# Performance work log

Measured on AMD Instinct MI355X. Metric: run time of the kernel, lower is better.

The kernel has to match this reference:

```python
import jax, jax.numpy as jnp
import numpy as np

DATA_SIZE = 16
OUT_DIM = 2 * DATA_SIZE  # predict_uncertainty=True
T = 128
BATCH = 4
L = 6368       # flattened root-MLP param count
H1 = 2133      # GradualMLP hidden 1: int(2/3*16 + 1/3*6368)
H2 = 4250      # GradualMLP hidden 2: int(1/3*16 + 2/3*6368)
FORCING_PROB = 1.0


def setup_inputs() -> dict:
    key = jax.random.key(0)
    k = jax.random.split(key, 8)
    xs = jax.random.normal(k[0], (BATCH, T, DATA_SIZE), jnp.float32)
    ts = jnp.broadcast_to(jnp.linspace(0.0, 1.0, T, dtype=jnp.float32), (BATCH, T))
    # A initialized near identity (module uses eye); small noise keeps the scan non-trivial but stable
    A = jnp.eye(L, dtype=jnp.float32) * 0.999 + 1e-4 * jax.random.normal(k[1], (L, L), jnp.float32)
    Bm = 0.01 * jax.random.normal(k[2], (L, DATA_SIZE + 1), jnp.float32)
    W1 = jax.random.normal(k[3], (H1, DATA_SIZE), jnp.float32) / np.float32(np.sqrt(DATA_SIZE))
    b1 = jnp.zeros((H1,), jnp.float32)
    W2 = jax.random.normal(k[4], (H2, H1), jnp.float32) / np.float32(np.sqrt(H1))
    b2 = jnp.zeros((H2,), jnp.float32)
    W3 = jax.random.normal(k[5], (L, H2), jnp.float32) / np.float32(np.sqrt(H2))
    b3 = jnp.zeros((L,), jnp.float32)
    return {"xs": xs, "ts": ts, "A": A, "Bm": Bm, "W1": W1, "b1": b1,
            "W2": W2, "b2": b2, "W3": W3, "b3": b3, "seed": 0}


def _root_apply(theta, tin):
    # unflatten theta into MLP(1 -> 64 -> 64 -> 32) params, in eqx leaf order (w, b per layer)
    w0 = theta[0:64].reshape(64, 1);      c0 = theta[64:128]
    w1 = theta[128:4224].reshape(64, 64); c1 = theta[4224:4288]
    w2 = theta[4288:6336].reshape(32, 64); c2 = theta[6336:6368]
    h = jax.nn.relu(w0 @ tin + c0)
    h = jaxax_relu = jax.nn.relu(w1 @ h + c1)
    out = w2 @ h + c2
    mean, std = jnp.split(out, 2)
    return jnp.concatenate([jnp.tanh(mean), jax.nn.softplus(std)])  # (OUT_DIM,)


def _forward_seq(xs_, ts_, k_, A, Bm, W1, b1, W2, b2, W3, b3):
    # theta_init = GradualMLP(data_size -> L) applied to xs_[0]
    h = jax.nn.relu(W1 @ xs_[0] + b1)
    h = jax.nn.relu(W2 @ h + b2)
    theta0 = W3 @ h + b3  # (L,)
    keys = jax.random.split(k_, xs_.shape[0])

    def f(carry, inp):
        thet, x_hat, x_prev, t_prev = carry
        x_true, t_curr, key = inp  # t_curr: (1,)
        delta_t = t_curr - t_prev
        x_t = jnp.where(jax.random.bernoulli(key, FORCING_PROB), x_true, x_hat)
        diff = jnp.concatenate([t_curr, x_t]) - jnp.concatenate([t_prev, x_prev])  # time_as_channel
        thet_next = A @ thet + Bm @ diff
        x_next = _root_apply(thet_next, t_curr + delta_t)
        return (thet_next, x_next[:DATA_SIZE], x_hat, t_curr), x_next

    _, xs_hat = jax.lax.scan(f, (theta0, xs_[0], xs_[0], ts_[0:1]), (xs_, ts_[:, None], keys))
    return xs_hat  # (T, OUT_DIM)


def reference(xs, ts, A, Bm, W1, b1, W2, b2, W3, b3, seed):
    ks = jax.random.split(jax.random.key(seed), xs.shape[0])
    fwd = lambda x_, t_, k_: _forward_seq(x_, t_, k_, A, Bm, W1, b1, W2, b2, W3, b3)
    return jax.vmap(fwd)(xs, ts, ks)  # (BATCH, T, OUT_DIM)
```

## Files before the change

### kernel.cpp

```cpp
#include <hip/hip_runtime.h>
#include <cmath>

#define T_STEPS 128
#define B_SZ    4
#define L_DIM   6368
#define L4V     1592
#define NCH     4
#define CH_SL   1592
#define CH_J    398
#define H1_DIM  2133
#define H2_DIM  4250
#define NBLK    256
#define NMV     255
#define NPAIR   3184

#define OFF_THA  0
#define OFF_THB  25472
#define OFF_W1T  50944
#define OFF_W2T  83712
#define OFF_DIFF 100096
#define OFF_H1   100236
#define OFF_H2   108768
#define OFF_CTR  125824

typedef __attribute__((address_space(1))) void gvoid;
typedef __attribute__((address_space(3))) void lvoid;

__device__ __forceinline__ void fma4(float4& acc, float4 a, float4 t0, float4 t1, float4 t2, float4 t3) {
    acc.x += a.x*t0.x + a.y*t1.x + a.z*t2.x + a.w*t3.x;
    acc.y += a.x*t0.y + a.y*t1.y + a.z*t2.y + a.w*t3.y;
    acc.z += a.x*t0.z + a.y*t1.z + a.z*t2.z + a.w*t3.z;
    acc.w += a.x*t0.w + a.y*t1.w + a.z*t2.w + a.w*t3.w;
}

__device__ __forceinline__ float4 red4(float4 v) {
    #pragma unroll
    for (int off = 32; off; off >>= 1) {
        v.x += __shfl_xor(v.x, off);
        v.y += __shfl_xor(v.y, off);
        v.z += __shfl_xor(v.z, off);
        v.w += __shfl_xor(v.w, off);
    }
    return v;
}

__device__ __forceinline__ void aux_write(float4* w1o, float4* w2o, int r, float4 v) {
    if (r >= 128 && r < 4224) {
        int j = r - 128;
        w1o[(j & 63)*64 + (j >> 6)] = v;
    } else if (r >= 4288 && r < 6336) {
        int j = r - 4288;
        w2o[(j & 63)*32 + (j >> 6)] = v;
    }
}

__device__ __forceinline__ float softplusf(float x) {
    return (x > 20.f) ? x : log1pf(expf(x));
}

__device__ __forceinline__ void grid_barrier(unsigned* ctr, int myc, unsigned it1) {
    __syncthreads();
    if (threadIdx.x == 0) {
        __threadfence();
        unsigned old = __hip_atomic_fetch_add(&ctr[myc*32], 1u,
                           __ATOMIC_RELAXED, __HIP_MEMORY_SCOPE_AGENT);
        if (old == it1*32u - 1u) {
            unsigned o2 = __hip_atomic_fetch_add(&ctr[8*32], 1u,
                              __ATOMIC_RELAXED, __HIP_MEMORY_SCOPE_AGENT);
            if (o2 == it1*8u - 1u) {
                #pragma unroll
                for (int c2 = 0; c2 < 8; ++c2)
                    __hip_atomic_store(&ctr[(9 + c2)*32], it1,
                        __ATOMIC_RELAXED, __HIP_MEMORY_SCOPE_AGENT);
            }
        }
        while (__hip_atomic_load(&ctr[(9 + myc)*32],
                   __ATOMIC_RELAXED, __HIP_MEMORY_SCOPE_AGENT) < it1)
            __builtin_amdgcn_s_sleep(8);
        __threadfence();
    }
    __syncthreads();
}

__device__ __forceinline__ void stage_issue(const float4* __restrict__ src, float4* dst,
                                            int w, int l, float4& tailv) {
    #pragma unroll
    for (int k = 0; k < 3; ++k) {
        const int p = k*512 + w*64 + l;
        const int q = p ^ ((p >> 3) & 7);
        __builtin_amdgcn_global_load_lds((gvoid*)(src + q),
                                         (lvoid*)(dst + k*512 + w*64), 16, 0, 0);
    }
    const int p = 1536 + w*7 + l;
    if (l < 7) tailv = src[p ^ ((p >> 3) & 7)];
}

__device__ __forceinline__ void stage_tail(float4* dst, int w, int l, float4 tailv) {
    if (l < 7) dst[1536 + w*7 + l] = tailv;
}

template<bool HB>
__device__ __forceinline__ void chunk_fma(const float4* __restrict__ a0, const float4* __restrict__ a1,
                                          const float4* __restrict__ c0, const float4* __restrict__ c1,
                                          const float4* __restrict__ sbuf, int jg0, int l,
                                          float4& A0, float4& A1, float4& B0, float4& B1)
{
    #pragma unroll
    for (int m = 0; m < 6; ++m) {
        const int jj = m*64 + l;
        const int jg = jg0 + jj;
        float4 av0 = a0[jg], av1 = a1[jg];
        float4 bv0, bv1;
        if (HB) { bv0 = c0[jg]; bv1 = c1[jg]; }
        const int sw = (jj >> 1) & 7;
        float4 t0 = sbuf[(4*jj + 0) ^ sw];
        float4 t1 = sbuf[(4*jj + 1) ^ sw];
        float4 t2 = sbuf[(4*jj + 2) ^ sw];
        float4 t3 = sbuf[(4*jj + 3) ^ sw];
        fma4(A0, av0, t0, t1, t2, t3);
        fma4(A1, av1, t0, t1, t2, t3);
        if (HB) {
            fma4(B0, bv0, t0, t1, t2, t3);
            fma4(B1, bv1, t0, t1, t2, t3);
        }
    }
    if (l < 14) {
        const int jj = 384 + l;
        const int jg = jg0 + jj;
        float4 av0 = a0[jg], av1 = a1[jg];
        float4 bv0, bv1;
        if (HB) { bv0 = c0[jg]; bv1 = c1[jg]; }
        const int sw = (jj >> 1) & 7;
        float4 t0 = sbuf[(4*jj + 0) ^ sw];
        float4 t1 = sbuf[(4*jj + 1) ^ sw];
        float4 t2 = sbuf[(4*jj + 2) ^ sw];
        float4 t3 = sbuf[(4*jj + 3) ^ sw];
        fma4(A0, av0, t0, t1, t2, t3);
        fma4(A1, av1, t0, t1, t2, t3);
        if (HB) {
            fma4(B0, bv0, t0, t1, t2, t3);
            fma4(B1, bv1, t0, t1, t2, t3);
        }
    }
}

__global__ __launch_bounds__(512, 2)
void seq_kernel(const float* __restrict__ A,
                const float* __restrict__ Bm,
                const float* __restrict__ xs,
                const float* __restrict__ ts,
                float* __restrict__ outp,
                float* thetaA, float* thetaB,
                float* w1t, float* w2t, float* diffb,
                unsigned* ctr)
{
    __shared__ float4 sth[2*CH_SL];
    const int blk = blockIdx.x;
    const int tid = threadIdx.x;
    const int w = tid >> 6, l = tid & 63;
    const int myc = blk & 7;
    const float4* A4 = (const float4*)A;

    if (blk < NMV) {
        const int p0 = (blk * NPAIR) / NMV;
        const int p1 = ((blk + 1) * NPAIR) / NMV;
        const int pA = p0 + w;
        const int pB = pA + 8;
        const bool hasB = pB < p1;
        const int rA = pA * 2;
        const int rB = pB * 2;
        const float4* a0 = A4 + (size_t)rA * L4V;
        const float4* a1 = a0 + L4V;
        const float4* c0 = A4 + (size_t)rB * L4V;
        const float4* c1 = c0 + L4V;

        float bmA0 = 0.f, bmA1 = 0.f, bmB0 = 0.f, bmB1 = 0.f;
        if (l < 17) {
            bmA0 = Bm[rA*17 + l];
            bmA1 = Bm[(rA + 1)*17 + l];
            if (hasB) { bmB0 = Bm[rB*17 + l]; bmB1 = Bm[(rB + 1)*17 + l]; }
        }

        for (int it = 0; it < T_STEPS; ++it) {
            const float4* thIn4 = (const float4*)((it & 1) ? thetaB : thetaA);
            float4* thOut4 = (float4*)((it & 1) ? thetaA : thetaB);
            float4* w1o = (float4*)(w1t + ((it + 1) & 1) * 16384);
            float4* w2o = (float4*)(w2t + ((it + 1) & 1) * 8192);
            const float* dvec = diffb + (it & 1) * 68;

            float e0 = 0.f, e1 = 0.f, e2 = 0.f, e3 = 0.f;
            if (l < 17) { e0 = dvec[l]; e1 = dvec[17 + l]; e2 = dvec[34 + l]; e3 = dvec[51 + l]; }
            float4 A0 = make_float4(bmA0*e0, bmA0*e1, bmA0*e2, bmA0*e3);
            float4 A1 = make_float4(bmA1*e0, bmA1*e1, bmA1*e2, bmA1*e3);
            float4 B0 = make_float4(bmB0*e0, bmB0*e1, bmB0*e2, bmB0*e3);
            float4 B1 = make_float4(bmB1*e0, bmB1*e1, bmB1*e2, bmB1*e3);

            float4 tailv;
            stage_issue(thIn4, sth, w, l, tailv);
            stage_tail(sth, w, l, tailv);
            __syncthreads();

            for (int c = 0; c < NCH; ++c) {
                if (c + 1 < NCH)
                    stage_issue(thIn4 + (c + 1)*CH_SL, sth + ((c + 1) & 1)*CH_SL, w, l, tailv);
                const float4* sbuf = sth + (c & 1)*CH_SL;
                if (hasB) chunk_fma<true >(a0, a1, c0, c1, sbuf, c*CH_J, l, A0, A1, B0, B1);
                else      chunk_fma<false>(a0, a1, c0, c1, sbuf, c*CH_J, l, A0, A1, B0, B1);
                if (c + 1 < NCH) {
                    stage_tail(sth + ((c + 1) & 1)*CH_SL, w, l, tailv);
                    __syncthreads();
                }
            }

            A0 = red4(A0); A1 = red4(A1);
            if (hasB) { B0 = red4(B0); B1 = red4(B1); }
            if (l == 0) {
                thOut4[rA]     = A0;  aux_write(w1o, w2o, rA,     A0);
                thOut4[rA + 1] = A1;  aux_write(w1o, w2o, rA + 1, A1);
                if (hasB) {
                    thOut4[rB]     = B0;  aux_write(w1o, w2o, rB,     B0);
                    thOut4[rB + 1] = B1;  aux_write(w1o, w2o, rB + 1, B1);
                }
            }
            grid_barrier(ctr, myc, (unsigned)(it + 1));
        }
    } else {
        const int b = w;
        for (int it = 0; it <= T_STEPS; ++it) {
            float xv = 0.f;
            if (b < B_SZ) {
                if (it >= 1) {
                    const int t = it - 1;
                    const float* th  = (it & 1) ? thetaB : thetaA;
                    const float* w1c = w1t + (it & 1) * 16384;
                    const float* w2c = w2t + (it & 1) * 8192;
                    float tcur = ts[b*T_STEPS + t];
                    float tin = (t >= 1) ? (2.f*tcur - ts[b*T_STEPS + t - 1]) : tcur;
                    float h0 = fmaxf(th[l*4 + b] * tin + th[(64 + l)*4 + b], 0.f);
                    float a1v = th[(4224 + l)*4 + b];
                    #pragma unroll
                    for (int k = 0; k < 64; ++k)
                        a1v += w1c[(k*64 + l)*4 + b] * __shfl(h0, k);
                    float h1 = fmaxf(a1v, 0.f);
                    float ov = th[(6336 + (l & 31))*4 + b];
                    #pragma unroll
                    for (int k = 0; k < 64; ++k)
                        ov += w2c[(k*32 + (l & 31))*4 + b] * __shfl(h1, k);
                    if (l < 32) {
                        xv = (l < 16) ? tanhf(ov) : softplusf(ov);
                        outp[(b*T_STEPS + t)*32 + l] = xv;
                    }
                }
                if (it + 1 <= T_STEPS - 1) {
                    float* dd = diffb + ((it + 1) & 1) * 68 + b*17;
                    if (l < 16) {
                        float xprev = (it >= 1) ? xv : xs[(size_t)(b*T_STEPS)*16 + l];
                        dd[1 + l] = xs[(size_t)(b*T_STEPS + it + 1)*16 + l] - xprev;
                    } else if (l == 16) {
                        dd[0] = ts[b*T_STEPS + it + 1] - ts[b*T_STEPS + it];
                    }
                }
            }
            if (it < T_STEPS) grid_barrier(ctr, myc, (unsigned)(it + 1));
        }
    }
}

__global__ __launch_bounds__(256)
void init_h1(const float* __restrict__ xs, const float* __restrict__ W1,
             const float* __restrict__ b1, float* __restrict__ h1ws,
             float* __restrict__ diffb, unsigned* __restrict__ ctr)
{
    const int b = blockIdx.y;
    const int r = blockIdx.x * 256 + threadIdx.x;
    if (blockIdx.x == 0 && b == 0) {
        if (threadIdx.x < 136) diffb[threadIdx.x] = 0.f;
        for (int z = threadIdx.x; z < 576; z += 256) ctr[z] = 0u;
    }
    if (r < H1_DIM) {
        const float* wr = W1 + r*16;
        const float* x0 = xs + (size_t)b * T_STEPS * 16;
        float s = b1[r];
        #pragma unroll
        for (int k = 0; k < 16; ++k) s += wr[k] * x0[k];
        h1ws[b*H1_DIM + r] = fmaxf(s, 0.f);
    }
}

__global__ __launch_bounds__(256)
void init_mm(const float* __restrict__ W, const float* __restrict__ bias,
             const float* __restrict__ in, float* __restrict__ outp,
             int rows, int K, int dorelu, int ilv)
{
    const int w = threadIdx.x >> 6, l = threadIdx.x & 63;
    const int gw = blockIdx.x * 4 + w;
    const int nw = gridDim.x * 4;
    for (int r = gw; r < rows; r += nw) {
        const float* wr = W + (size_t)r * K;
        float a0 = 0.f, a1 = 0.f, a2 = 0.f, a3 = 0.f;
        for (int k = l; k < K; k += 64) {
            float wv = wr[k];
            a0 += wv * in[k];
            a1 += wv * in[K + k];
            a2 += wv * in[2*K + k];
            a3 += wv * in[3*K + k];
        }
        #pragma unroll
        for (int off = 32; off; off >>= 1) {
            a0 += __shfl_xor(a0, off);
            a1 += __shfl_xor(a1, off);
            a2 += __shfl_xor(a2, off);
            a3 += __shfl_xor(a3, off);
        }
        if (l == 0) {
            float bb = bias[r];
            a0 += bb; a1 += bb; a2 += bb; a3 += bb;
            if (dorelu) {
                a0 = fmaxf(a0, 0.f); a1 = fmaxf(a1, 0.f);
                a2 = fmaxf(a2, 0.f); a3 = fmaxf(a3, 0.f);
            }
            if (ilv) {
                outp[r*4 + 0] = a0; outp[r*4 + 1] = a1;
                outp[r*4 + 2] = a2; outp[r*4 + 3] = a3;
            } else {
                outp[0*rows + r] = a0; outp[1*rows + r] = a1;
                outp[2*rows + r] = a2; outp[3*rows + r] = a3;
            }
        }
    }
}

extern "C" void kernel_launch(void* const* d_in, const int* in_sizes, int n_in,
                              void* d_out, int out_size, void* d_ws, size_t ws_size,
                              hipStream_t stream) {
    const float* xs = (const float*)d_in[0];
    const float* ts = (const float*)d_in[1];
    const float* A  = (const float*)d_in[2];
    const float* Bm = (const float*)d_in[3];
    const float* W1 = (const float*)d_in[4];
    const float* b1 = (const float*)d_in[5];
    const float* W2 = (const float*)d_in[6];
    const float* b2 = (const float*)d_in[7];
    const float* W3 = (const float*)d_in[8];
    const float* b3 = (const float*)d_in[9];
    float* outp = (float*)d_out;
    float* wsf  = (float*)d_ws;

    float* thetaA = wsf + OFF_THA;
    float* thetaB = wsf + OFF_THB;
    float* w1t    = wsf + OFF_W1T;
    float* w2t    = wsf + OFF_W2T;
    float* diffb  = wsf + OFF_DIFF;
    float* h1ws   = wsf + OFF_H1;
    float* h2ws   = wsf + OFF_H2;
    unsigned* ctr = (unsigned*)(wsf + OFF_CTR);

    init_h1<<<dim3((H1_DIM + 255)/256, B_SZ), 256, 0, stream>>>(xs, W1, b1, h1ws, diffb, ctr);
    init_mm<<<dim3(128), 256, 0, stream>>>(W2, b2, h1ws, h2ws, H2_DIM, H1_DIM, 1, 0);
    init_mm<<<dim3(256), 256, 0, stream>>>(W3, b3, h2ws, thetaA, L_DIM, H2_DIM, 0, 1);
    seq_kernel<<<dim3(NBLK), dim3(512), 0, stream>>>(A, Bm, xs, ts, outp,
                                                     thetaA, thetaB, w1t, w2t, diffb, ctr);
}
```

Before: 5.041 ms.

## Software-pipeline A-row loads across chunks with register prefetch and two larger theta stages

Restructures the per-step matvec so theta is staged in two halves instead of four chunks, which removes two block barriers per step. Each thread keeps six float4 A-row values per row in registers and reloads the next group while doing the current FMAs, so global loads overlap with compute, including across time steps. The tail columns of each row are loaded once before the loop and kept in registers. Launch bounds drop to one block per CU because of the higher register use, and the grid-barrier spin sleep is shortened.

```diff
diff --git a/kernel.cpp b/kernel.cpp
--- a/kernel.cpp
+++ b/kernel.cpp
@@ -5,9 +5,8 @@
 #define B_SZ    4
 #define L_DIM   6368
 #define L4V     1592
-#define NCH     4
-#define CH_SL   1592
-#define CH_J    398
+#define CH_SL   3184
+#define CH_J    796
 #define H1_DIM  2133
 #define H2_DIM  4250
 #define NBLK    256
@@ -76,75 +75,91 @@
         }
         while (__hip_atomic_load(&ctr[(9 + myc)*32],
                    __ATOMIC_RELAXED, __HIP_MEMORY_SCOPE_AGENT) < it1)
-            __builtin_amdgcn_s_sleep(8);
+            __builtin_amdgcn_s_sleep(2);
         __threadfence();
     }
     __syncthreads();
 }
 
 __device__ __forceinline__ void stage_issue(const float4* __restrict__ src, float4* dst,
-                                            int w, int l, float4& tailv) {
+                                            int tid, int w, int l, float4& tailv) {
     #pragma unroll
-    for (int k = 0; k < 3; ++k) {
+    for (int k = 0; k < 6; ++k) {
         const int p = k*512 + w*64 + l;
         const int q = p ^ ((p >> 3) & 7);
         __builtin_amdgcn_global_load_lds((gvoid*)(src + q),
                                          (lvoid*)(dst + k*512 + w*64), 16, 0, 0);
     }
-    const int p = 1536 + w*7 + l;
-    if (l < 7) tailv = src[p ^ ((p >> 3) & 7)];
-}
-
-__device__ __forceinline__ void stage_tail(float4* dst, int w, int l, float4 tailv) {
-    if (l < 7) dst[1536 + w*7 + l] = tailv;
+    const int p = 3072 + tid;
+    if (tid < 112) tailv = src[p ^ ((p >> 3) & 7)];
+}
+
+__device__ __forceinline__ void stage_tail(float4* dst, int tid, float4 tailv) {
+    if (tid < 112) dst[3072 + tid] = tailv;
 }
 
 template<bool HB>
-__device__ __forceinline__ void chunk_fma(const float4* __restrict__ a0, const float4* __restrict__ a1,
-                                          const float4* __restrict__ c0, const float4* __restrict__ c1,
-                                          const float4* __restrict__ sbuf, int jg0, int l,
-                                          float4& A0, float4& A1, float4& B0, float4& B1)
+__device__ __forceinline__ void load6(const float4* __restrict__ a0, const float4* __restrict__ a1,
+                                      const float4* __restrict__ c0, const float4* __restrict__ c1,
+                                      int jg0, int l,
+                                      float4 (&r0)[6], float4 (&r1)[6],
+                                      float4 (&s0)[6], float4 (&s1)[6])
 {
     #pragma unroll
     for (int m = 0; m < 6; ++m) {
-        const int jj = m*64 + l;
-        const int jg = jg0 + jj;
-        float4 av0 = a0[jg], av1 = a1[jg];
-        float4 bv0, bv1;
-        if (HB) { bv0 = c0[jg]; bv1 = c1[jg]; }
+        const int jg = jg0 + m*64 + l;
+        r0[m] = a0[jg]; r1[m] = a1[jg];
+        if (HB) { s0[m] = c0[jg]; s1[m] = c1[jg]; }
+    }
+}
+
+template<bool HB>
+__device__ __forceinline__ void cons6_refill(const float4* __restrict__ a0, const float4* __restrict__ a1,
+                                             const float4* __restrict__ c0, const float4* __restrict__ c1,
+                                             const float4* __restrict__ sbuf, int js0, int refill_jg0, int l,
+                                             float4 (&r0)[6], float4 (&r1)[6],
+                                             float4 (&s0)[6], float4 (&s1)[6],
+                                             float4& A0, float4& A1, float4& B0, float4& B1)
+{
+    #pragma unroll
+    for (int m = 0; m < 6; ++m) {
+        const int jj = js0 + m*64 + l;
         const int sw = (jj >> 1) & 7;
         float4 t0 = sbuf[(4*jj + 0) ^ sw];
         float4 t1 = sbuf[(4*jj + 1) ^ sw];
         float4 t2 = sbuf[(4*jj + 2) ^ sw];
         float4 t3 = sbuf[(4*jj + 3) ^ sw];
+        float4 av0 = r0[m], av1 = r1[m];
+        float4 bv0, bv1;
+        if (HB) { bv0 = s0[m]; bv1 = s1[m]; }
+        const int jg = refill_jg0 + m*64 + l;
+        r0[m] = a0[jg]; r1[m] = a1[jg];
+        if (HB) { s0[m] = c0[jg]; s1[m] = c1[jg]; }
         fma4(A0, av0, t0, t1, t2, t3);
         fma4(A1, av1, t0, t1, t2, t3);
-        if (HB) {
-            fma4(B0, bv0, t0, t1, t2, t3);
-            fma4(B1, bv1, t0, t1, t2, t3);
-        }
-    }
-    if (l < 14) {
-        const int jj = 384 + l;
-        const int jg = jg0 + jj;
-        float4 av0 = a0[jg], av1 = a1[jg];
-        float4 bv0, bv1;
-        if (HB) { bv0 = c0[jg]; bv1 = c1[jg]; }
+        if (HB) { fma4(B0, bv0, t0, t1, t2, t3); fma4(B1, bv1, t0, t1, t2, t3); }
+    }
+}
+
+template<bool HB>
+__device__ __forceinline__ void cons_tail(const float4* __restrict__ sbuf, int l, bool tl,
+                                          float4 u0, float4 u1, float4 v0, float4 v1,
+                                          float4& A0, float4& A1, float4& B0, float4& B1)
+{
+    if (tl) {
+        const int jj = 768 + l;
         const int sw = (jj >> 1) & 7;
         float4 t0 = sbuf[(4*jj + 0) ^ sw];
         float4 t1 = sbuf[(4*jj + 1) ^ sw];
         float4 t2 = sbuf[(4*jj + 2) ^ sw];
         float4 t3 = sbuf[(4*jj + 3) ^ sw];
-        fma4(A0, av0, t0, t1, t2, t3);
-        fma4(A1, av1, t0, t1, t2, t3);
-        if (HB) {
-            fma4(B0, bv0, t0, t1, t2, t3);
-            fma4(B1, bv1, t0, t1, t2, t3);
-        }
-    }
-}
-
-__global__ __launch_bounds__(512, 2)
+        fma4(A0, u0, t0, t1, t2, t3);
+        fma4(A1, u1, t0, t1, t2, t3);
+        if (HB) { fma4(B0, v0, t0, t1, t2, t3); fma4(B1, v1, t0, t1, t2, t3); }
+    }
+}
+
+__global__ __launch_bounds__(512, 1)
 void seq_kernel(const float* __restrict__ A,
                 const float* __restrict__ Bm,
                 const float* __restrict__ xs,
@@ -181,6 +196,21 @@
             if (hasB) { bmB0 = Bm[rB*17 + l]; bmB1 = Bm[(rB + 1)*17 + l]; }
         }
 
+        const bool tl = l < 28;
+        float4 ua0, ua1, va0, va1, ub0, ub1, vb0, vb1;
+        if (tl) {
+            ua0 = a0[768 + l];  ua1 = a1[768 + l];
+            ub0 = a0[1564 + l]; ub1 = a1[1564 + l];
+            if (hasB) {
+                va0 = c0[768 + l];  va1 = c1[768 + l];
+                vb0 = c0[1564 + l]; vb1 = c1[1564 + l];
+            }
+        }
+
+        float4 r0[6], r1[6], s0[6], s1[6];
+        if (hasB) load6<true >(a0, a1, c0, c1, 0, l, r0, r1, s0, s1);
+        else      load6<false>(a0, a1, c0, c1, 0, l, r0, r1, s0, s1);
+
         for (int it = 0; it < T_STEPS; ++it) {
             const float4* thIn4 = (const float4*)((it & 1) ? thetaB : thetaA);
             float4* thOut4 = (float4*)((it & 1) ? thetaA : thetaB);
@@ -195,21 +225,32 @@
             float4 B0 = make_float4(bmB0*e0, bmB0*e1, bmB0*e2, bmB0*e3);
             float4 B1 = make_float4(bmB1*e0, bmB1*e1, bmB1*e2, bmB1*e3);
 
-            float4 tailv;
-            stage_issue(thIn4, sth, w, l, tailv);
-            stage_tail(sth, w, l, tailv);
+            float4 tv0, tv1;
+            stage_issue(thIn4, sth, tid, w, l, tv0);
+            stage_tail(sth, tid, tv0);
             __syncthreads();
 
-            for (int c = 0; c < NCH; ++c) {
-                if (c + 1 < NCH)
-                    stage_issue(thIn4 + (c + 1)*CH_SL, sth + ((c + 1) & 1)*CH_SL, w, l, tailv);
-                const float4* sbuf = sth + (c & 1)*CH_SL;
-                if (hasB) chunk_fma<true >(a0, a1, c0, c1, sbuf, c*CH_J, l, A0, A1, B0, B1);
-                else      chunk_fma<false>(a0, a1, c0, c1, sbuf, c*CH_J, l, A0, A1, B0, B1);
-                if (c + 1 < NCH) {
-                    stage_tail(sth + ((c + 1) & 1)*CH_SL, w, l, tailv);
-                    __syncthreads();
-                }
+            stage_issue(thIn4 + CH_SL, sth + CH_SL, tid, w, l, tv1);
+            if (hasB) {
+                cons6_refill<true >(a0,a1,c0,c1, sth, 0,   384,  l, r0,r1,s0,s1, A0,A1,B0,B1);
+                cons6_refill<true >(a0,a1,c0,c1, sth, 384, 796,  l, r0,r1,s0,s1, A0,A1,B0,B1);
+                cons_tail<true >(sth, l, tl, ua0, ua1, va0, va1, A0, A1, B0, B1);
+            } else {
+                cons6_refill<false>(a0,a1,c0,c1, sth, 0,   384,  l, r0,r1,s0,s1, A0,A1,B0,B1);
+                cons6_refill<false>(a0,a1,c0,c1, sth, 384, 796,  l, r0,r1,s0,s1, A0,A1,B0,B1);
+                cons_tail<false>(sth, l, tl, ua0, ua1, va0, va1, A0, A1, B0, B1);
+            }
+            stage_tail(sth + CH_SL, tid, tv1);
+            __syncthreads();
+
+            if (hasB) {
+                cons6_refill<true >(a0,a1,c0,c1, sth + CH_SL, 0,   1180, l, r0,r1,s0,s1, A0,A1,B0,B1);
+                cons6_refill<true >(a0,a1,c0,c1, sth + CH_SL, 384, 0,    l, r0,r1,s0,s1, A0,A1,B0,B1);
+                cons_tail<true >(sth + CH_SL, l, tl, ub0, ub1, vb0, vb1, A0, A1, B0, B1);
+            } else {
+                cons6_refill<false>(a0,a1,c0,c1, sth + CH_SL, 0,   1180, l, r0,r1,s0,s1, A0,A1,B0,B1);
+                cons6_refill<false>(a0,a1,c0,c1, sth + CH_SL, 384, 0,    l, r0,r1,s0,s1, A0,A1,B0,B1);
+                cons_tail<false>(sth + CH_SL, l, tl, ub0, ub1, vb0, vb1, A0, A1, B0, B1);
             }
 
             A0 = red4(A0); A1 = red4(A1);
```

Result: slower. 11.51 ms (+128.3%).
